# Kernel tuning notes

Hardware: AMD Instinct MI355X
Metric: run time of the kernel (lower is better)

Reference implementation:

```python
import jax, jax.numpy as jnp
import numpy as np

EPS = 1e-5
DN = ('NCHW', 'OIHW', 'NCHW')

def conv(x, w, b, stride, pad):
    y = jax.lax.conv_general_dilated(x, w, (stride, stride), [(pad, pad), (pad, pad)], dimension_numbers=DN)
    return y + b[None, :, None, None]

def instance_norm(x, gamma, beta):
    # normalize over spatial dims per (N, C)
    mu = jnp.mean(x, axis=(2, 3), keepdims=True)
    var = jnp.var(x, axis=(2, 3), keepdims=True)
    xh = (x - mu) * jax.lax.rsqrt(var + EPS)
    return xh * gamma[None, :, None, None] + beta[None, :, None, None]

def lrelu(x):
    return jnp.where(x >= 0, x, 0.2 * x)

def block(x, w, b, g, be, stride, pad):
    return lrelu(instance_norm(conv(x, w, b, stride, pad), g, be))

def setup_inputs() -> dict:
    key = jax.random.key(0)
    ks = jax.random.split(key, 16)
    dim = 64
    def rn(k, shape, s=0.05):
        return jax.random.normal(k, shape, dtype=jnp.float32) * s
    inp = {
        'x':   jax.random.normal(ks[0], (256, 3, 64, 64), dtype=jnp.float32),
        'w1': rn(ks[1], (dim, 3, 5, 5)),        'b1': jnp.zeros((dim,), jnp.float32),
        'g1': jnp.ones((dim,), jnp.float32),    'be1': jnp.zeros((dim,), jnp.float32),
        'w2': rn(ks[2], (dim*2, dim, 5, 5)),    'b2': jnp.zeros((dim*2,), jnp.float32),
        'g2': jnp.ones((dim*2,), jnp.float32),  'be2': jnp.zeros((dim*2,), jnp.float32),
        'w3': rn(ks[3], (dim*4, dim*2, 5, 5)),  'b3': jnp.zeros((dim*4,), jnp.float32),
        'g3': jnp.ones((dim*4,), jnp.float32),  'be3': jnp.zeros((dim*4,), jnp.float32),
        'w4': rn(ks[4], (dim*4, dim*4, 3, 3)),  'b4': jnp.zeros((dim*4,), jnp.float32),
        'g4': jnp.ones((dim*4,), jnp.float32),  'be4': jnp.zeros((dim*4,), jnp.float32),
        # MBD tensor T: (in_features=4096, out_features=64, kernel_dims=50), init N(0,1)
        'T':  jax.random.normal(ks[5], (4096, 64, 50), dtype=jnp.float32),
        'fc_w': rn(ks[6], (1000, 4096 + 64), s=0.02),
        'fc_b': jnp.zeros((1000,), jnp.float32),
    }
    return inp

def reference(x, w1, b1, g1, be1, w2, b2, g2, be2, w3, b3, g3, be3, w4, b4, g4, be4, T, fc_w, fc_b):
    bs = x.shape[0]
    f = block(x, w1, b1, g1, be1, 2, 2)   # (bs,64,32,32)
    f = block(f, w2, b2, g2, be2, 2, 2)   # (bs,128,16,16)
    f = block(f, w3, b3, g3, be3, 2, 2)   # (bs,256,8,8)
    f = block(f, w4, b4, g4, be4, 2, 1)   # (bs,256,4,4)
    feat = f.reshape(bs, -1)              # (bs,4096)
    # minibatch discrimination
    M = jnp.einsum('bi,iok->bok', feat, T)          # (bs,64,50)
    norm = jnp.sum(jnp.abs(M[None] - M[:, None]), axis=3)  # (bs,bs,64); [i,j]=|M_i-M_j|
    o_b = jnp.sum(jnp.exp(-norm), axis=0) - 1.0     # (bs,64)
    mb = jnp.concatenate([feat, o_b], axis=1)       # (bs,4160)
    y = mb @ fc_w.T + fc_b                          # (bs,1000)
    return feat, y
```

## Files before the change

### kernel.cpp

```cpp
#include <hip/hip_runtime.h>
#include <hip/hip_fp16.h>
#include <math.h>

#define EPSF 1e-5f

typedef __attribute__((ext_vector_type(4))) float  floatx4;
typedef __attribute__((ext_vector_type(4))) short  short4v;
typedef __attribute__((ext_vector_type(8))) short  short8v;

__device__ __forceinline__ unsigned short cvt_bf16(float f){
  unsigned u = __float_as_uint(f);
  unsigned r = (u + 0x7FFFu + ((u >> 16) & 1u)) >> 16;
  return (unsigned short)r;
}
__device__ __forceinline__ float bf2f(unsigned short h){
  return __uint_as_float(((unsigned)h) << 16);
}
__device__ __forceinline__ short8v ld_frag(const unsigned short* p){
  short4v lo = *(const short4v*)p;
  short4v hi = *(const short4v*)(p + 4);
  return __builtin_shufflevector(lo, hi, 0,1,2,3,4,5,6,7);
}
__device__ __forceinline__ float lrelu(float x){ return x >= 0.f ? x : 0.2f*x; }

__global__ __launch_bounds__(256) void prep_k(const float* __restrict__ w1, const float* __restrict__ w2,
                                              const float* __restrict__ w3, const float* __restrict__ w4,
                                              unsigned short* __restrict__ wb1, unsigned short* __restrict__ wb2,
                                              unsigned short* __restrict__ wb3, unsigned short* __restrict__ wb4,
                                              float* __restrict__ SQ){
  int b = blockIdx.x, t = threadIdx.x;
  if (b < 32){
    int idx = b*256 + t;
    int j = idx&7, lane = (idx>>3)&63, ks = (idx>>9)&3, grp = idx>>11;
    int co = grp*16 + (lane&15);
    int k = ks*32 + ((lane>>4)<<3) + j;
    int tap6 = k>>2, ci = k&3;
    int kh = tap6/6, kw = tap6 - kh*6;
    float v = 0.f;
    if (ci < 3 && kh < 5 && kw < 5) v = w1[(co*3 + ci)*25 + kh*5 + kw];
    wb1[idx] = cvt_bf16(v);
  } else if (b < 832){
    int idx = (b-32)*256 + t;
    int grp = idx/25600, rem = idx - grp*25600;
    int tap = rem/1024, rem2 = rem - tap*1024;
    int ccg = rem2>>9, lane = (rem2>>3)&63, j = rem2&7;
    int co = grp*16 + (lane&15);
    int ci = ccg*32 + ((lane>>4)<<3) + j;
    wb2[idx] = cvt_bf16(w2[(co*64 + ci)*25 + tap]);
  } else if (b < 4032){
    int idx = (b-832)*256 + t;
    int grp = idx/51200, rem = idx - grp*51200;
    int tap = rem/2048, rem2 = rem - tap*2048;
    int ccg = rem2>>9, lane = (rem2>>3)&63, j = rem2&7;
    int co = grp*16 + (lane&15);
    int ci = ccg*32 + ((lane>>4)<<3) + j;
    wb3[idx] = cvt_bf16(w3[(co*128 + ci)*25 + tap]);
  } else if (b < 6336){
    int idx = (b-4032)*256 + t;
    int grp = idx/36864, rem = idx - grp*36864;
    int tap = rem/4096, rem2 = rem - tap*4096;
    int ccg = rem2>>9, lane = (rem2>>3)&63, j = rem2&7;
    int co = grp*16 + (lane&15);
    int ci = ccg*32 + ((lane>>4)<<3) + j;
    wb4[idx] = cvt_bf16(w4[(co*256 + ci)*9 + tap]);
  } else {
    int idx = (b-6336)*256 + t;
    SQ[idx] = 0.f;
  }
}

__global__ __launch_bounds__(256) void packT_k(const float* __restrict__ T,
                                               unsigned short* __restrict__ Tp){
  const int b = blockIdx.x, t = threadIdx.x;
  __shared__ float tile[32][133];
  const int nb = b % 25, kt = b / 25;
  const int n0 = nb*128, k0 = kt*32;
  #pragma unroll
  for (int m=0;m<4;m++){
    int idx = m*256 + t;
    int row = idx>>5, c4 = (idx&31)<<2;
    const float4 v = *(const float4*)&T[(k0+row)*3200 + n0 + c4];
    tile[row][c4]   = v.x; tile[row][c4+1] = v.y;
    tile[row][c4+2] = v.z; tile[row][c4+3] = v.w;
  }
  __syncthreads();
  #pragma unroll
  for (int m=0;m<2;m++){
    int c = m*256 + t;
    int ngl = c>>6, lane = c&63, q = lane>>4, r = lane&15;
    unsigned short h[8];
    #pragma unroll
    for (int j=0;j<8;j++) h[j] = cvt_bf16(tile[q*8+j][ngl*16 + r]);
    *(uint4*)&Tp[(((nb*8 + ngl)*128 + kt)*64 + lane)*8] = *(const uint4*)h;
  }
}

__global__ __launch_bounds__(256) void packW_k(const float* __restrict__ W,
                                               unsigned short* __restrict__ Wp){
  int idx = blockIdx.x*256 + threadIdx.x;
  int lane = idx & 63, rem = idx >> 6;
  int kt = rem % 130, ng = rem / 130;
  int q = lane>>4, r = lane&15;
  int orow = ng*16 + r, k = kt*32 + (q<<3);
  unsigned short h[8] = {0,0,0,0,0,0,0,0};
  if (orow < 1000){
    float4 v0 = *(const float4*)&W[orow*4160 + k];
    float4 v1 = *(const float4*)&W[orow*4160 + k + 4];
    h[0]=cvt_bf16(v0.x); h[1]=cvt_bf16(v0.y); h[2]=cvt_bf16(v0.z); h[3]=cvt_bf16(v0.w);
    h[4]=cvt_bf16(v1.x); h[5]=cvt_bf16(v1.y); h[6]=cvt_bf16(v1.z); h[7]=cvt_bf16(v1.w);
  }
  *(uint4*)&Wp[idx*8] = *(const uint4*)h;
}

__global__ __launch_bounds__(256) void conv1_k(const float* __restrict__ x, const unsigned short* __restrict__ wb1P,
                                               float* __restrict__ S1, float* __restrict__ Q1,
                                               unsigned short* __restrict__ f1raw){
  const int t = threadIdx.x, n = blockIdx.x>>1, half = blockIdx.x&1;
  const int w = t>>6, lane = t&63, q = lane>>4, l16 = lane&15;
  __shared__ __align__(16) unsigned short img[36*68*4];
  short8v bf[4][4];
  #pragma unroll
  for (int nt=0;nt<4;nt++)
    #pragma unroll
    for (int ks=0;ks<4;ks++)
      bf[nt][ks] = *(const short8v*)&wb1P[((nt*4+ks)*64 + lane)*8];
  for (int i=t; i<4896; i+=256) ((unsigned*)img)[i] = 0u;
  __syncthreads();
  for (int idx=t; idx<1680; idx+=256){
    int ci = idx/560, rem = idx - ci*560;
    int tih = rem>>4, iw4 = (rem&15)<<2;
    int ih = half*32 - 2 + tih;
    if ((unsigned)ih < 64u){
      float4 v = *(const float4*)&x[((n*3+ci)<<12) + (ih<<6) + iw4];
      int base = (tih*68 + iw4 + 2)*4 + ci;
      img[base]    = cvt_bf16(v.x);
      img[base+4]  = cvt_bf16(v.y);
      img[base+8]  = cvt_bf16(v.z);
      img[base+12] = cvt_bf16(v.w);
    }
  }
  __syncthreads();
  floatx4 acc[8][4];
  #pragma unroll
  for (int mi=0;mi<8;mi++)
    #pragma unroll
    for (int nt=0;nt<4;nt++) acc[mi][nt] = (floatx4){0.f,0.f,0.f,0.f};
  #pragma unroll
  for (int mi=0; mi<8; mi++){
    int r = w*8 + mi;
    int ohl = r>>1, ow = ((r&1)<<4) + l16;
    #pragma unroll
    for (int ks=0; ks<4; ks++){
      int t0 = ks*8 + 2*q;
      int kh = t0/6, kw = t0 - kh*6;
      short8v a = ld_frag(&img[((ohl*2+kh)*68 + ow*2 + kw)*4]);
      #pragma unroll
      for (int nt=0; nt<4; nt++)
        acc[mi][nt] = __builtin_amdgcn_mfma_f32_16x16x32_bf16(a, bf[nt][ks], acc[mi][nt], 0,0,0);
    }
  }
  float sreg[4] = {0,0,0,0}, qreg[4] = {0,0,0,0};
  #pragma unroll
  for (int mi=0;mi<8;mi++){
    int r = w*8 + mi;
    #pragma unroll
    for (int nt=0;nt<4;nt++)
      #pragma unroll
      for (int e=0;e<4;e++){
        float v = acc[mi][nt][e];
        sreg[nt] += v; qreg[nt] += v*v;
        int px = half*512 + (r<<4) + (q<<2) + e;
        f1raw[(((n<<10)+px)<<6) + (nt<<4) + l16] = cvt_bf16(v);
      }
  }
  #pragma unroll
  for (int nt=0;nt<4;nt++){
    float s = sreg[nt], qq = qreg[nt];
    s  += __shfl_xor(s,16,64);  s  += __shfl_xor(s,32,64);
    qq += __shfl_xor(qq,16,64); qq += __shfl_xor(qq,32,64);
    if (q==0){
      atomicAdd(&S1[(n<<6) + (nt<<4) + l16], s);
      atomicAdd(&Q1[(n<<6) + (nt<<4) + l16], qq);
    }
  }
}

__global__ __launch_bounds__(512) void conv2_k(const unsigned short* __restrict__ fin,
                                               const unsigned short* __restrict__ wbP,
                                               const float* __restrict__ S1, const float* __restrict__ Q1,
                                               const float* __restrict__ g1, const float* __restrict__ be1,
                                               float* __restrict__ S2, float* __restrict__ Q2,
                                               unsigned short* __restrict__ fout){
  const int t = threadIdx.x;
  const int n = blockIdx.x >> 1, half = blockIdx.x & 1;
  const int w = t>>6, lane = t&63, q = lane>>4, l16 = lane&15;
  const int rw = w&1, cw = w>>1;
  __shared__ __align__(16) unsigned short tile[684*40];
  __shared__ float gmA[64], btA[64];
  if (t < 64){
    float S = S1[(n<<6)+t], Q = Q1[(n<<6)+t];
    float mu = S*(1.f/1024.f), var = fmaxf(Q*(1.f/1024.f) - mu*mu, 0.f);
    float r = rsqrtf(var+EPSF)*g1[t];
    gmA[t] = r; btA[t] = be1[t] - mu*r;
  }
  __syncthreads();
  floatx4 acc[4][2];
  #pragma unroll
  for (int mt=0;mt<4;mt++)
    #pragma unroll
    for (int nt=0;nt<2;nt++) acc[mt][nt] = (floatx4){0.f,0.f,0.f,0.f};
  int cellb[4];
  #pragma unroll
  for (int mt=0;mt<4;mt++){
    int r = rw*64 + mt*16 + l16;
    int ohl = r>>4, ow = r&15;
    cellb[mt] = (2*ohl)*36 + 2*ow;
  }
  for (int ccg = 0; ccg < 2; ccg++){
    const int cc = ccg<<5;
    if (ccg) __syncthreads();
    #pragma unroll
    for (int it=0; it<6; it++){
      int idx = it*512 + t;
      if (idx < 2736){
        int cell = idx>>2, ci0 = (idx&3)<<3;
        int tih = cell/36, tiw = cell - tih*36;
        int ih = half*16 + tih - 2, iw = tiw - 2;
        uint4 v = {0u,0u,0u,0u};
        if ((unsigned)ih < 32u && (unsigned)iw < 32u){
          v = *(const uint4*)&fin[(((n*32+ih)*32 + iw)<<6) + cc + ci0];
          unsigned short* hp = (unsigned short*)&v;
          #pragma unroll
          for (int jj=0;jj<8;jj++){
            int c = cc + ci0 + jj;
            hp[jj] = cvt_bf16(lrelu(bf2f(hp[jj])*gmA[c]+btA[c]));
          }
        }
        *(uint4*)&tile[cell*40 + ci0] = v;
      }
    }
    __syncthreads();
    const unsigned short* bp[2];
    #pragma unroll
    for (int nt=0;nt<2;nt++)
      bp[nt] = wbP + ((((cw*2+nt)*25)*2 + ccg)<<9) + lane*8;
    short8v bq[2][4];
    #pragma unroll
    for (int p=0;p<4;p++)
      #pragma unroll
      for (int nt=0;nt<2;nt++) bq[nt][p] = *(const short8v*)(bp[nt] + (p<<10));
    short8v acur[4];
    #pragma unroll
    for (int mt=0;mt<4;mt++) acur[mt] = *(const short8v*)&tile[cellb[mt]*40 + q*8];
    #pragma unroll
    for (int tap=0; tap<25; tap++){
      short8v anx[4];
      if (tap+1 < 25){
        const int t1 = tap+1, kh1 = t1/5, kw1 = t1 - kh1*5;
        const int aoff1 = kh1*36 + kw1;
        #pragma unroll
        for (int mt=0;mt<4;mt++) anx[mt] = *(const short8v*)&tile[(cellb[mt]+aoff1)*40 + q*8];
      }
      #pragma unroll
      for (int mt=0;mt<4;mt++)
        #pragma unroll
        for (int nt=0;nt<2;nt++)
          acc[mt][nt] = __builtin_amdgcn_mfma_f32_16x16x32_bf16(acur[mt], bq[nt][tap&3], acc[mt][nt], 0,0,0);
      if (tap+4 < 25){
        #pragma unroll
        for (int nt=0;nt<2;nt++) bq[nt][tap&3] = *(const short8v*)(bp[nt] + ((tap+4)<<10));
      }
      if (tap+1 < 25){
        #pragma unroll
        for (int mt=0;mt<4;mt++) acur[mt] = anx[mt];
      }
    }
  }
  #pragma unroll
  for (int nt=0;nt<2;nt++){
    int co = cw*32 + nt*16 + l16;
    float s=0.f, qq=0.f;
    #pragma unroll
    for (int mt=0;mt<4;mt++)
      #pragma unroll
      for (int e=0;e<4;e++){ float xv = acc[mt][nt][e]; s += xv; qq += xv*xv; }
    s  += __shfl_xor(s,16,64);  s  += __shfl_xor(s,32,64);
    qq += __shfl_xor(qq,16,64); qq += __shfl_xor(qq,32,64);
    if (q == 0){
      atomicAdd(&S2[n*128 + co], s);
      atomicAdd(&Q2[n*128 + co], qq);
    }
    #pragma unroll
    for (int mt=0;mt<4;mt++)
      #pragma unroll
      for (int e=0;e<4;e++){
        int px = half*128 + rw*64 + mt*16 + q*4 + e;
        fout[((n<<8) + px)*128 + co] = cvt_bf16(acc[mt][nt][e]);
      }
  }
}

__global__ __launch_bounds__(512) void conv3_k(const unsigned short* __restrict__ fin,
                                               const unsigned short* __restrict__ wbP,
                                               const float* __restrict__ S2, const float* __restrict__ Q2,
                                               const float* __restrict__ g2, const float* __restrict__ be2,
                                               const float* __restrict__ g, const float* __restrict__ be,
                                               unsigned short* __restrict__ fout){
  const int t = threadIdx.x, n = blockIdx.x, co0 = blockIdx.y<<7;
  const int w = t>>6, lane = t&63, q = lane>>4, l16 = lane&15;
  const int rw = w&1, cw = w>>1;
  __shared__ __align__(16) unsigned short tile[361*40];
  __shared__ float gmA[128], btA[128];
  __shared__ float SQs[2][128], SQq[2][128];
  if (t < 128){
    float S = S2[n*128+t], Q = Q2[n*128+t];
    float mu = S*(1.f/256.f), var = fmaxf(Q*(1.f/256.f) - mu*mu, 0.f);
    float r = rsqrtf(var+EPSF)*g2[t];
    gmA[t] = r; btA[t] = be2[t] - mu*r;
  }
  __syncthreads();
  floatx4 acc[2][2];
  #pragma unroll
  for (int mt=0;mt<2;mt++)
    #pragma unroll
    for (int nt=0;nt<2;nt++) acc[mt][nt] = (floatx4){0.f,0.f,0.f,0.f};
  int cellb[2];
  #pragma unroll
  for (int mt=0;mt<2;mt++){
    int r = rw*32 + mt*16 + l16;
    int oh = r>>3, ow = r&7;
    cellb[mt] = (2*oh)*19 + 2*ow;
  }
  for (int ccg = 0; ccg < 4; ccg++){
    const int cc = ccg<<5;
    if (ccg) __syncthreads();
    #pragma unroll
    for (int it=0; it<3; it++){
      int idx = it*512 + t;
      if (idx < 1444){
        int cell = idx>>2, ci0 = (idx&3)<<3;
        int tih = cell/19, tiw = cell - tih*19;
        int ih = tih - 2, iw = tiw - 2;
        uint4 v = {0u,0u,0u,0u};
        if ((unsigned)ih < 16u && (unsigned)iw < 16u){
          v = *(const uint4*)&fin[(((n*16+ih)*16 + iw)<<7) + cc + ci0];
          unsigned short* hp = (unsigned short*)&v;
          #pragma unroll
          for (int jj=0;jj<8;jj++){
            int c = cc + ci0 + jj;
            hp[jj] = cvt_bf16(lrelu(bf2f(hp[jj])*gmA[c]+btA[c]));
          }
        }
        *(uint4*)&tile[cell*40 + ci0] = v;
      }
    }
    __syncthreads();
    const unsigned short* bp[2];
    #pragma unroll
    for (int nt=0;nt<2;nt++)
      bp[nt] = wbP + (((((co0>>4)+cw*2+nt)*25)*4 + ccg)<<9) + lane*8;
    short8v bq[2][4];
    #pragma unroll
    for (int p=0;p<4;p++)
      #pragma unroll
      for (int nt=0;nt<2;nt++) bq[nt][p] = *(const short8v*)(bp[nt] + (p<<11));
    short8v acur[2];
    #pragma unroll
    for (int mt=0;mt<2;mt++) acur[mt] = *(const short8v*)&tile[cellb[mt]*40 + q*8];
    #pragma unroll
    for (int tap=0; tap<25; tap++){
      short8v anx[2];
      if (tap+1 < 25){
        const int t1 = tap+1, kh1 = t1/5, kw1 = t1 - kh1*5;
        const int aoff1 = kh1*19 + kw1;
        #pragma unroll
        for (int mt=0;mt<2;mt++) anx[mt] = *(const short8v*)&tile[(cellb[mt]+aoff1)*40 + q*8];
      }
      #pragma unroll
      for (int mt=0;mt<2;mt++)
        #pragma unroll
        for (int nt=0;nt<2;nt++)
          acc[mt][nt] = __builtin_amdgcn_mfma_f32_16x16x32_bf16(acur[mt], bq[nt][tap&3], acc[mt][nt], 0,0,0);
      if (tap+4 < 25){
        #pragma unroll
        for (int nt=0;nt<2;nt++) bq[nt][tap&3] = *(const short8v*)(bp[nt] + ((tap+4)<<11));
      }
      if (tap+1 < 25){
        #pragma unroll
        for (int mt=0;mt<2;mt++) acur[mt] = anx[mt];
      }
    }
  }
  #pragma unroll
  for (int nt=0;nt<2;nt++){
    int lcol = cw*32 + nt*16 + l16;
    float s=0.f, qq=0.f;
    #pragma unroll
    for (int mt=0;mt<2;mt++)
      #pragma unroll
      for (int e=0;e<4;e++){ float xv = acc[mt][nt][e]; s += xv; qq += xv*xv; }
    s  += __shfl_xor(s,16,64);  s  += __shfl_xor(s,32,64);
    qq += __shfl_xor(qq,16,64); qq += __shfl_xor(qq,32,64);
    if (q == 0){ SQs[rw][lcol] = s; SQq[rw][lcol] = qq; }
  }
  __syncthreads();
  #pragma unroll
  for (int nt=0;nt<2;nt++){
    int lcol = cw*32 + nt*16 + l16, co = co0 + lcol;
    float S = SQs[0][lcol] + SQs[1][lcol];
    float Q = SQq[0][lcol] + SQq[1][lcol];
    float mu = S*(1.f/64.f), var = fmaxf(Q*(1.f/64.f) - mu*mu, 0.f);
    float gmv = rsqrtf(var+EPSF)*g[co];
    float btv = be[co] - mu*gmv;
    #pragma unroll
    for (int mt=0;mt<2;mt++)
      #pragma unroll
      for (int e=0;e<4;e++){
        int row = rw*32 + mt*16 + q*4 + e;
        fout[((n<<6) + row)*256 + co] = cvt_bf16(lrelu(acc[mt][nt][e]*gmv+btv));
      }
  }
}

__global__ __launch_bounds__(256) void conv4_k(const unsigned short* __restrict__ fin,
                                               const unsigned short* __restrict__ wbP,
                                               const float* __restrict__ g, const float* __restrict__ be,
                                               float* __restrict__ feat, unsigned short* __restrict__ featb){
  const int t = threadIdx.x;
  const int n0 = blockIdx.x << 1, co0 = blockIdx.y << 6;
  const int w = t>>6, lane = t&63, q = lane>>4, l16 = lane&15;
  const int rw = w&1, cw = w>>1;
  __shared__ __align__(16) unsigned short tile[2*81*40];
  floatx4 acc[2];
  acc[0] = (floatx4){0.f,0.f,0.f,0.f};
  acc[1] = (floatx4){0.f,0.f,0.f,0.f};
  const int oh = l16>>2, ow = l16&3;
  const int cellb = (2*oh)*9 + 2*ow;
  for (int ccg = 0; ccg < 8; ccg++){
    const int cc = ccg<<5;
    if (ccg) __syncthreads();
    #pragma unroll
    for (int it=0; it<3; it++){
      int idx = it*256 + t;
      if (idx < 648){
        int img = idx >= 324 ? 1 : 0;
        int rem = idx - img*324;
        int cell = rem>>2, ci0 = (rem&3)<<3;
        int tih = cell/9, tiw = cell - tih*9;
        int ih = tih - 1, iw = tiw - 1;
        uint4 v = {0u,0u,0u,0u};
        if ((unsigned)ih < 8u && (unsigned)iw < 8u)
          v = *(const uint4*)&fin[((((n0+img)*8+ih)*8 + iw)<<8) + cc + ci0];
        *(uint4*)&tile[(img*81+cell)*40 + ci0] = v;
      }
    }
    __syncthreads();
    const unsigned short* bp[2];
    #pragma unroll
    for (int nt=0;nt<2;nt++)
      bp[nt] = wbP + (((((co0>>4)+cw*2+nt)*9)*8 + ccg)<<9) + lane*8;
    short8v bq[2][4];
    #pragma unroll
    for (int p=0;p<4;p++)
      #pragma unroll
      for (int nt=0;nt<2;nt++) bq[nt][p] = *(const short8v*)(bp[nt] + (p<<12));
    #pragma unroll
    for (int tap=0; tap<9; tap++){
      const int kh = tap/3, kw = tap - kh*3;
      short8v a = *(const short8v*)&tile[(rw*81 + cellb + kh*9 + kw)*40 + q*8];
      #pragma unroll
      for (int nt=0;nt<2;nt++)
        acc[nt] = __builtin_amdgcn_mfma_f32_16x16x32_bf16(a, bq[nt][tap&3], acc[nt], 0,0,0);
      if (tap+4 < 9){
        #pragma unroll
        for (int nt=0;nt<2;nt++) bq[nt][tap&3] = *(const short8v*)(bp[nt] + ((tap+4)<<12));
      }
    }
  }
  const int nn = n0 + rw;
  #pragma unroll
  for (int nt=0;nt<2;nt++){
    int co = co0 + cw*32 + nt*16 + l16;
    float s=0.f, qq=0.f;
    #pragma unroll
    for (int e=0;e<4;e++){ float xv = acc[nt][e]; s += xv; qq += xv*xv; }
    s  += __shfl_xor(s,16,64);  s  += __shfl_xor(s,32,64);
    qq += __shfl_xor(qq,16,64); qq += __shfl_xor(qq,32,64);
    float mu = s*(1.f/16.f), var = fmaxf(qq*(1.f/16.f) - mu*mu, 0.f);
    float gmv = rsqrtf(var+EPSF)*g[co];
    float btv = be[co] - mu*gmv;
    #pragma unroll
    for (int e=0;e<4;e++){
      int px = q*4 + e;
      float vv = lrelu(acc[nt][e]*gmv+btv);
      feat [(nn<<12) + (co<<4) + px] = vv;
      featb[(nn<<12) + (co<<4) + px] = cvt_bf16(vv);
    }
  }
}

__global__ __launch_bounds__(256) void gemmM_k(const unsigned short* __restrict__ A,
                                               const unsigned short* __restrict__ Tp,
                                               float* __restrict__ Cp){
  const int t = threadIdx.x;
  const int n0 = blockIdx.x<<7, b0 = blockIdx.y<<7, k0 = blockIdx.z<<9;
  const int w = t>>6, lane = t&63, q = lane>>4, l16 = lane&15;
  const int rw = w&1, cw = w>>1;
  floatx4 acc[4][4];
  #pragma unroll
  for (int mt=0;mt<4;mt++)
    #pragma unroll
    for (int nt=0;nt<4;nt++) acc[mt][nt] = (floatx4){0.f,0.f,0.f,0.f};
  const unsigned short* Ab[4];
  const unsigned short* Bb[4];
  #pragma unroll
  for (int mt=0;mt<4;mt++)
    Ab[mt] = A + (b0 + (rw<<6) + (mt<<4) + l16)*4096 + k0 + (q<<3);
  #pragma unroll
  for (int nt=0;nt<4;nt++)
    Bb[nt] = Tp + ((((n0>>4) + (cw<<2) + nt)*128 + (k0>>5))*64 + lane)*8;
  #pragma unroll 4
  for (int kt=0; kt<16; kt++){
    short8v af[4], bfr[4];
    #pragma unroll
    for (int mt=0;mt<4;mt++) af[mt] = *(const short8v*)(Ab[mt] + kt*32);
    #pragma unroll
    for (int nt=0;nt<4;nt++) bfr[nt] = *(const short8v*)(Bb[nt] + kt*512);
    #pragma unroll
    for (int mt=0;mt<4;mt++)
      #pragma unroll
      for (int nt=0;nt<4;nt++)
        acc[mt][nt] = __builtin_amdgcn_mfma_f32_16x16x32_bf16(af[mt], bfr[nt], acc[mt][nt], 0,0,0);
  }
  float* C = Cp + blockIdx.z * 819200;
  #pragma unroll
  for (int mt=0;mt<4;mt++)
    #pragma unroll
    for (int nt=0;nt<4;nt++)
      #pragma unroll
      for (int e=0;e<4;e++){
        int row = b0 + (rw<<6) + (mt<<4) + (q<<2) + e;
        int col = n0 + (cw<<6) + (nt<<4) + l16;
        C[row*3200 + col] = acc[mt][nt][e];
      }
}

__global__ __launch_bounds__(256) void reduceM_k(const float* __restrict__ Cp, __half* __restrict__ Mh){
  int idx = blockIdx.x*256 + threadIdx.x;
  if (idx >= 917504) return;
  int i = idx / 3584, r = idx - i*3584;
  int o = r / 56, k = r - o*56;
  float v = 0.f;
  if (k < 50){
    int src = i*3200 + o*50 + k;
    #pragma unroll
    for (int s = 0; s < 8; s++) v += Cp[s*819200 + src];
  }
  Mh[idx] = __float2half(v);
}

__global__ __launch_bounds__(256) void pairv2_k(const __half* __restrict__ Mh,
                                                float* __restrict__ obp){
  const int t = threadIdx.x, jb = blockIdx.x, ib = blockIdx.y;
  const int o = t & 63, jj = t >> 6;
  const int j = jb*4 + jj;
  const uint4* M4 = (const uint4*)Mh;
  uint4 mj[7];
  #pragma unroll
  for (int u=0;u<7;u++) mj[u] = M4[j*448 + o*7 + u];
  const int i0 = ib*32;
  uint4 cur[7], nxt[7];
  #pragma unroll
  for (int u=0;u<7;u++) cur[u] = M4[i0*448 + o*7 + u];
  float sum = 0.f;
  for (int ii=0; ii<32; ii++){
    if (ii < 31){
      #pragma unroll
      for (int u=0;u<7;u++) nxt[u] = M4[(i0+ii+1)*448 + o*7 + u];
    }
    __half2 a0 = __float2half2_rn(0.f), a1 = a0, a2 = a0, a3 = a0;
    #pragma unroll
    for (int u=0;u<7;u++){
      const __half2* ah = (const __half2*)&cur[u];
      const __half2* bh = (const __half2*)&mj[u];
      a0 = __hadd2(a0, __habs2(__hsub2(ah[0], bh[0])));
      a1 = __hadd2(a1, __habs2(__hsub2(ah[1], bh[1])));
      a2 = __hadd2(a2, __habs2(__hsub2(ah[2], bh[2])));
      a3 = __hadd2(a3, __habs2(__hsub2(ah[3], bh[3])));
    }
    __half2 s01 = __hadd2(a0, a1), s23 = __hadd2(a2, a3);
    __half2 s = __hadd2(s01, s23);
    float dsum = __low2float(s) + __high2float(s);
    sum += __expf(-dsum);
    #pragma unroll
    for (int u=0;u<7;u++) cur[u] = nxt[u];
  }
  obp[ib*16384 + jb*256 + t] = sum;
}

__global__ __launch_bounds__(256) void finalizeOB_k(const float* __restrict__ obp,
                                                    unsigned short* __restrict__ obb){
  int idx = blockIdx.x*256 + threadIdx.x;
  float v = -1.0f;
  #pragma unroll
  for (int s=0;s<8;s++) v += obp[s*16384 + idx];
  obb[idx] = cvt_bf16(v);
}

__global__ __launch_bounds__(256) void gemmFC_k(const unsigned short* __restrict__ featb,
                                                const unsigned short* __restrict__ obb,
                                                const unsigned short* __restrict__ Wp,
                                                float* __restrict__ Cp){
  const int t = threadIdx.x;
  const int o0 = blockIdx.x<<7, b0 = blockIdx.y<<7, kz = blockIdx.z;
  const int w = t>>6, lane = t&63, q = lane>>4, l16 = lane&15;
  const int rw = w&1, cw = w>>1;
  floatx4 acc[4][4];
  #pragma unroll
  for (int mt=0;mt<4;mt++)
    #pragma unroll
    for (int nt=0;nt<4;nt++) acc[mt][nt] = (floatx4){0.f,0.f,0.f,0.f};
  int rowb[4];
  #pragma unroll
  for (int mt=0;mt<4;mt++) rowb[mt] = b0 + (rw<<6) + (mt<<4) + l16;
  const unsigned short* Bb[4];
  #pragma unroll
  for (int nt=0;nt<4;nt++)
    Bb[nt] = Wp + ((((o0>>4) + (cw<<2) + nt)*130 + kz*10)*64 + lane)*8;
  #pragma unroll 2
  for (int kt=0; kt<10; kt++){
    int k = kz*320 + kt*32 + (q<<3);
    short8v af[4], bfr[4];
    #pragma unroll
    for (int mt=0;mt<4;mt++)
      af[mt] = (k < 4096) ? *(const short8v*)&featb[rowb[mt]*4096 + k]
                          : *(const short8v*)&obb[rowb[mt]*64 + (k-4096)];
    #pragma unroll
    for (int nt=0;nt<4;nt++) bfr[nt] = *(const short8v*)(Bb[nt] + kt*512);
    #pragma unroll
    for (int mt=0;mt<4;mt++)
      #pragma unroll
      for (int nt=0;nt<4;nt++)
        acc[mt][nt] = __builtin_amdgcn_mfma_f32_16x16x32_bf16(af[mt], bfr[nt], acc[mt][nt], 0,0,0);
  }
  float* C = Cp + blockIdx.z * 256000;
  #pragma unroll
  for (int mt=0;mt<4;mt++)
    #pragma unroll
    for (int nt=0;nt<4;nt++)
      #pragma unroll
      for (int e=0;e<4;e++){
        int row = b0 + (rw<<6) + (mt<<4) + (q<<2) + e;
        int col = o0 + (cw<<6) + (nt<<4) + l16;
        if (col < 1000) C[row*1000 + col] = acc[mt][nt][e];
      }
}

__global__ __launch_bounds__(256) void reduceY_k(const float* __restrict__ Cp, const float* __restrict__ bias,
                                                 float* __restrict__ y){
  int idx = blockIdx.x * 256 + threadIdx.x;
  if (idx >= 256000) return;
  int o = idx % 1000;
  float r = bias[o];
  #pragma unroll
  for (int s = 0; s < 13; s++) r += Cp[s*256000 + idx];
  y[idx] = r;
}

extern "C" void kernel_launch(void* const* d_in, const int* in_sizes, int n_in,
                              void* d_out, int out_size, void* d_ws, size_t ws_size,
                              hipStream_t stream){
  const float* x   = (const float*)d_in[0];
  const float* w1  = (const float*)d_in[1];
  const float* g1  = (const float*)d_in[3];
  const float* be1 = (const float*)d_in[4];
  const float* w2  = (const float*)d_in[5];
  const float* g2  = (const float*)d_in[7];
  const float* be2 = (const float*)d_in[8];
  const float* w3  = (const float*)d_in[9];
  const float* g3  = (const float*)d_in[11];
  const float* be3 = (const float*)d_in[12];
  const float* w4  = (const float*)d_in[13];
  const float* g4  = (const float*)d_in[15];
  const float* be4 = (const float*)d_in[16];
  const float* T   = (const float*)d_in[17];
  const float* fcw = (const float*)d_in[18];
  const float* fcb = (const float*)d_in[19];
  float* out = (float*)d_out;
  float* ws  = (float*)d_ws;

  unsigned short* f1raw = (unsigned short*)ws;
  unsigned short* Tp    = (unsigned short*)ws;
  unsigned short* f2    = (unsigned short*)(ws + 8388608);
  unsigned short* f3    = (unsigned short*)(ws + 12582912);
  unsigned short* featb = (unsigned short*)(ws + 14680064);
  unsigned short* wb1   = (unsigned short*)(ws + 15204352);
  unsigned short* wb2   = (unsigned short*)(ws + 15208448);
  unsigned short* wb3   = (unsigned short*)(ws + 15310848);
  unsigned short* wb4   = (unsigned short*)(ws + 15720448);
  float* S1    = ws + 16015360;
  float* Q1    = ws + 16031744;
  float* S2    = ws + 16048128;
  float* Q2    = ws + 16080896;
  float* Mp    = ws + 16113664;
  unsigned short* Wp  = (unsigned short*)(ws + 16113664);
  __half* Mh   = (__half*)(ws + 22667264);
  unsigned short* obb = (unsigned short*)(ws + 23142400);
  float* yp    = ws + 23150592;
  float* obp   = ws + 26478592;
  float* feat  = out;
  float* y     = out + 1048576;

  prep_k<<<dim3(6720), 256, 0, stream>>>(w1, w2, w3, w4, wb1, wb2, wb3, wb4, S1);

  conv1_k<<<dim3(512),     256, 0, stream>>>(x, wb1, S1, Q1, f1raw);
  conv2_k<<<dim3(512),     512, 0, stream>>>(f1raw, wb2, S1, Q1, g1, be1, S2, Q2, f2);
  packT_k<<<dim3(3200),    256, 0, stream>>>(T, Tp);
  conv3_k<<<dim3(256, 2),  512, 0, stream>>>(f2, wb3, S2, Q2, g2, be2, g3, be3, f3);
  conv4_k<<<dim3(128, 4),  256, 0, stream>>>(f3, wb4, g4, be4, feat, featb);

  gemmM_k  <<<dim3(25, 2, 8),  256, 0, stream>>>(featb, Tp, Mp);
  reduceM_k<<<dim3(3584),      256, 0, stream>>>(Mp, Mh);
  packW_k  <<<dim3(2080),      256, 0, stream>>>(fcw, Wp);
  pairv2_k <<<dim3(64, 8),     256, 0, stream>>>(Mh, obp);
  finalizeOB_k<<<dim3(64),     256, 0, stream>>>(obp, obb);
  gemmFC_k <<<dim3(8, 2, 13),  256, 0, stream>>>(featb, obb, Wp, yp);
  reduceY_k<<<dim3(1000),      256, 0, stream>>>(yp, fcb, y);
}
```

Baseline: 329.8 us.

## Double-buffer conv3 input tile and prefetch next channel group during MFMA loop

In conv3, the single LDS tile becomes two buffers. The next 32-channel group is loaded from global memory into registers before the MFMA tap loop and normalized and written into the other buffer afterward, so each step needs one barrier instead of two and the global load latency overlaps compute. In both conv2 and conv3, the explicit one-tap-ahead LDS A-fragment prefetch is removed and each tap's fragments are loaded directly, leaving scheduling to the compiler. Doubling the LDS tile (about 58KB total) and holding the prefetched registers may reduce occupancy.

```diff
diff --git a/kernel.cpp b/kernel.cpp
--- a/kernel.cpp
+++ b/kernel.cpp
@@ -249,30 +249,21 @@
     for (int p=0;p<4;p++)
       #pragma unroll
       for (int nt=0;nt<2;nt++) bq[nt][p] = *(const short8v*)(bp[nt] + (p<<10));
-    short8v acur[4];
-    #pragma unroll
-    for (int mt=0;mt<4;mt++) acur[mt] = *(const short8v*)&tile[cellb[mt]*40 + q*8];
     #pragma unroll
     for (int tap=0; tap<25; tap++){
-      short8v anx[4];
-      if (tap+1 < 25){
-        const int t1 = tap+1, kh1 = t1/5, kw1 = t1 - kh1*5;
-        const int aoff1 = kh1*36 + kw1;
-        #pragma unroll
-        for (int mt=0;mt<4;mt++) anx[mt] = *(const short8v*)&tile[(cellb[mt]+aoff1)*40 + q*8];
-      }
+      const int kh = tap/5, kw = tap - kh*5;
+      const int aoff = kh*36 + kw;
+      short8v a[4];
+      #pragma unroll
+      for (int mt=0;mt<4;mt++) a[mt] = *(const short8v*)&tile[(cellb[mt]+aoff)*40 + q*8];
       #pragma unroll
       for (int mt=0;mt<4;mt++)
         #pragma unroll
         for (int nt=0;nt<2;nt++)
-          acc[mt][nt] = __builtin_amdgcn_mfma_f32_16x16x32_bf16(acur[mt], bq[nt][tap&3], acc[mt][nt], 0,0,0);
+          acc[mt][nt] = __builtin_amdgcn_mfma_f32_16x16x32_bf16(a[mt], bq[nt][tap&3], acc[mt][nt], 0,0,0);
       if (tap+4 < 25){
         #pragma unroll
         for (int nt=0;nt<2;nt++) bq[nt][tap&3] = *(const short8v*)(bp[nt] + ((tap+4)<<10));
-      }
-      if (tap+1 < 25){
-        #pragma unroll
-        for (int mt=0;mt<4;mt++) acur[mt] = anx[mt];
       }
     }
   }
@@ -309,7 +300,7 @@
   const int t = threadIdx.x, n = blockIdx.x, co0 = blockIdx.y<<7;
   const int w = t>>6, lane = t&63, q = lane>>4, l16 = lane&15;
   const int rw = w&1, cw = w>>1;
-  __shared__ __align__(16) unsigned short tile[361*40];
+  __shared__ __align__(16) unsigned short tile[2][14440];
   __shared__ float gmA[128], btA[128];
   __shared__ float SQs[2][128], SQq[2][128];
   if (t < 128){
@@ -319,6 +310,35 @@
     gmA[t] = r; btA[t] = be2[t] - mu*r;
   }
   __syncthreads();
+  int scell[3], sci0[3], sbase[3]; bool sinb[3], svalid[3];
+  #pragma unroll
+  for (int it=0;it<3;it++){
+    int idx = it*512 + t;
+    svalid[it] = idx < 1444;
+    int cell = idx>>2, ci0 = (idx&3)<<3;
+    int tih = cell/19, tiw = cell - tih*19;
+    int ih = tih - 2, iw = tiw - 2;
+    scell[it] = cell; sci0[it] = ci0;
+    sinb[it] = svalid[it] && (unsigned)ih < 16u && (unsigned)iw < 16u;
+    sbase[it] = (((n*16+ih)*16 + iw)<<7) + ci0;
+  }
+  #pragma unroll
+  for (int it=0;it<3;it++){
+    if (svalid[it]){
+      uint4 v = {0u,0u,0u,0u};
+      if (sinb[it]){
+        v = *(const uint4*)&fin[sbase[it]];
+        unsigned short* hp = (unsigned short*)&v;
+        #pragma unroll
+        for (int jj=0;jj<8;jj++){
+          int c = sci0[it] + jj;
+          hp[jj] = cvt_bf16(lrelu(bf2f(hp[jj])*gmA[c]+btA[c]));
+        }
+      }
+      *(uint4*)&tile[0][scell[it]*40 + sci0[it]] = v;
+    }
+  }
+  __syncthreads();
   floatx4 acc[2][2];
   #pragma unroll
   for (int mt=0;mt<2;mt++)
@@ -332,29 +352,16 @@
     cellb[mt] = (2*oh)*19 + 2*ow;
   }
   for (int ccg = 0; ccg < 4; ccg++){
-    const int cc = ccg<<5;
-    if (ccg) __syncthreads();
-    #pragma unroll
-    for (int it=0; it<3; it++){
-      int idx = it*512 + t;
-      if (idx < 1444){
-        int cell = idx>>2, ci0 = (idx&3)<<3;
-        int tih = cell/19, tiw = cell - tih*19;
-        int ih = tih - 2, iw = tiw - 2;
-        uint4 v = {0u,0u,0u,0u};
-        if ((unsigned)ih < 16u && (unsigned)iw < 16u){
-          v = *(const uint4*)&fin[(((n*16+ih)*16 + iw)<<7) + cc + ci0];
-          unsigned short* hp = (unsigned short*)&v;
-          #pragma unroll
-          for (int jj=0;jj<8;jj++){
-            int c = cc + ci0 + jj;
-            hp[jj] = cvt_bf16(lrelu(bf2f(hp[jj])*gmA[c]+btA[c]));
-          }
-        }
-        *(uint4*)&tile[cell*40 + ci0] = v;
-      }
-    }
-    __syncthreads();
+    uint4 regs[3];
+    if (ccg < 3){
+      const int cc = (ccg+1)<<5;
+      #pragma unroll
+      for (int it=0;it<3;it++){
+        regs[it] = (uint4){0u,0u,0u,0u};
+        if (sinb[it]) regs[it] = *(const uint4*)&fin[sbase[it] + cc];
+      }
+    }
+    const unsigned short* tb = tile[ccg&1];
     const unsigned short* bp[2];
     #pragma unroll
     for (int nt=0;nt<2;nt++)
@@ -364,32 +371,43 @@
     for (int p=0;p<4;p++)
       #pragma unroll
       for (int nt=0;nt<2;nt++) bq[nt][p] = *(const short8v*)(bp[nt] + (p<<11));
-    short8v acur[2];
-    #pragma unroll
-    for (int mt=0;mt<2;mt++) acur[mt] = *(const short8v*)&tile[cellb[mt]*40 + q*8];
     #pragma unroll
     for (int tap=0; tap<25; tap++){
-      short8v anx[2];
-      if (tap+1 < 25){
-        const int t1 = tap+1, kh1 = t1/5, kw1 = t1 - kh1*5;
-        const int aoff1 = kh1*19 + kw1;
-        #pragma unroll
-        for (int mt=0;mt<2;mt++) anx[mt] = *(const short8v*)&tile[(cellb[mt]+aoff1)*40 + q*8];
-      }
+      const int kh = tap/5, kw = tap - kh*5;
+      const int aoff = kh*19 + kw;
+      short8v a[2];
+      #pragma unroll
+      for (int mt=0;mt<2;mt++) a[mt] = *(const short8v*)&tb[(cellb[mt]+aoff)*40 + q*8];
       #pragma unroll
       for (int mt=0;mt<2;mt++)
         #pragma unroll
         for (int nt=0;nt<2;nt++)
-          acc[mt][nt] = __builtin_amdgcn_mfma_f32_16x16x32_bf16(acur[mt], bq[nt][tap&3], acc[mt][nt], 0,0,0);
+          acc[mt][nt] = __builtin_amdgcn_mfma_f32_16x16x32_bf16(a[mt], bq[nt][tap&3], acc[mt][nt], 0,0,0);
       if (tap+4 < 25){
         #pragma unroll
         for (int nt=0;nt<2;nt++) bq[nt][tap&3] = *(const short8v*)(bp[nt] + ((tap+4)<<11));
       }
-      if (tap+1 < 25){
-        #pragma unroll
-        for (int mt=0;mt<2;mt++) acur[mt] = anx[mt];
-      }
-    }
+    }
+    if (ccg < 3){
+      const int cc = (ccg+1)<<5;
+      unsigned short* tw = tile[(ccg+1)&1];
+      #pragma unroll
+      for (int it=0;it<3;it++){
+        if (svalid[it]){
+          uint4 v = regs[it];
+          if (sinb[it]){
+            unsigned short* hp = (unsigned short*)&v;
+            #pragma unroll
+            for (int jj=0;jj<8;jj++){
+              int c = cc + sci0[it] + jj;
+              hp[jj] = cvt_bf16(lrelu(bf2f(hp[jj])*gmA[c]+btA[c]));
+            }
+          }
+          *(uint4*)&tw[scell[it]*40 + sci0[it]] = v;
+        }
+      }
+    }
+    __syncthreads();
   }
   #pragma unroll
   for (int nt=0;nt<2;nt++){
```

Result: no change. 336.2 us (+1.9%).
